# Kernel tuning notes

Measured on AMD Instinct MI355X. Metric: run time of the kernel, lower is better.

Reference implementation:

```python
import jax, jax.numpy as jnp
import numpy as np

V = 50000   # vocab_size
E = 300     # embed_dim (GRU input size)
H = 256     # hidden_dim
R = 2048    # number of replies
L0 = 128    # original content length
LR = 64     # max reply length (padded)

def setup_inputs() -> dict:
    key = jax.random.key(0)
    ks = jax.random.split(key, 20)
    s = 0.05
    inp = {
        "original_tokens": jax.random.randint(ks[0], (L0,), 0, V),
        "reply_tokens":    jax.random.randint(ks[1], (R, LR), 0, V),
        "reply_lengths":   jax.random.randint(ks[2], (R,), 1, LR + 1),
        "label":           jax.random.uniform(ks[3], (1,), dtype=jnp.float32),
        # learned params
        "embed": jax.random.normal(ks[4], (V, E), dtype=jnp.float32) * s,
        # bi-GRU forward direction (PyTorch layout: gates [r, z, n] stacked)
        "Wih_f": jax.random.normal(ks[5], (3 * H, E), dtype=jnp.float32) * s,
        "Whh_f": jax.random.normal(ks[6], (3 * H, H), dtype=jnp.float32) * s,
        "bih_f": jax.random.normal(ks[7], (3 * H,), dtype=jnp.float32) * s,
        "bhh_f": jax.random.normal(ks[8], (3 * H,), dtype=jnp.float32) * s,
        # bi-GRU reverse direction
        "Wih_b": jax.random.normal(ks[9], (3 * H, E), dtype=jnp.float32) * s,
        "Whh_b": jax.random.normal(ks[10], (3 * H, H), dtype=jnp.float32) * s,
        "bih_b": jax.random.normal(ks[11], (3 * H,), dtype=jnp.float32) * s,
        "bhh_b": jax.random.normal(ks[12], (3 * H,), dtype=jnp.float32) * s,
        # self.linear : 2H -> H
        "Wl": jax.random.normal(ks[13], (H, 2 * H), dtype=jnp.float32) * s,
        "bl": jax.random.normal(ks[14], (H,), dtype=jnp.float32) * s,
        # self.output_linear : H -> 1 (batch_size = 1)
        "Wo": jax.random.normal(ks[15], (1, H), dtype=jnp.float32) * s,
        "bo": jax.random.normal(ks[16], (1,), dtype=jnp.float32) * s,
    }
    return inp


def _gru_dir(x, Wih, Whh, bih, bhh):
    """Single-direction GRU over x: (S, E) -> (ys: (S, H), hT: (H,)).
    PyTorch gate math: r,z,n with n = tanh(gi_n + r * gh_n)."""
    def step(h, xt):
        gi = Wih @ xt + bih            # (3H,)
        gh = Whh @ h + bhh             # (3H,)
        r = jax.nn.sigmoid(gi[:H] + gh[:H])
        z = jax.nn.sigmoid(gi[H:2 * H] + gh[H:2 * H])
        n = jnp.tanh(gi[2 * H:] + r * gh[2 * H:])
        h_new = (1.0 - z) * n + z * h
        return h_new, h_new
    h0 = jnp.zeros((H,), dtype=x.dtype)
    hT, ys = jax.lax.scan(step, h0, x)
    return ys, hT


def reference(original_tokens, reply_tokens, reply_lengths, label,
              embed, Wih_f, Whh_f, bih_f, bhh_f,
              Wih_b, Whh_b, bih_b, bhh_b, Wl, bl, Wo, bo):
    # per-event embedding + sum pooling (batched replacement of Python loop)
    orig = embed[original_tokens].sum(axis=0)                      # (E,)
    mask = (jnp.arange(LR)[None, :] < reply_lengths[:, None]).astype(embed.dtype)
    rep = jnp.einsum('rle,rl->re', embed[reply_tokens], mask)      # (R, E)
    X = jnp.concatenate([orig[None, :], rep], axis=0)              # (S, E), S = R+1

    # bidirectional GRU (batch dim is 1, squeezed)
    ys_f, h_f = _gru_dir(X, Wih_f, Whh_f, bih_f, bhh_f)            # (S, H), (H,)
    ys_b, h_b = _gru_dir(X[::-1], Wih_b, Whh_b, bih_b, bhh_b)
    ys_b = ys_b[::-1]                                              # (S, H)

    out2 = jnp.concatenate([ys_f, ys_b], axis=-1)                  # (S, 2H)
    output = out2 @ Wl.T + bl                                      # (S, H)

    # hidden = sum over directions of final hidden states
    hsum = h_f + h_b                                               # (H,)

    # dot-product attention: query = hsum, keys = values = output
    scores = output @ hsum                                         # (S,)
    w = jax.nn.softmax(scores)                                     # attention dist
    ctx = w @ output                                               # (H,)

    result = jax.nn.sigmoid(ctx @ Wo.T + bo)                       # (1,)
    loss = (label - result) ** 2                                   # (1,)
    return (output[:, None, :], loss, result)                      # output: (S,1,H)
```

## Files before the change

kernel.cpp:

```cpp
#include <hip/hip_runtime.h>
#include <cstdint>
#include <cstddef>

#define NV 50000
#define NE 300
#define NH 256
#define NR 2048
#define NL0 128
#define NLR 64
#define NS 2049
#define G3 768

static constexpr size_t alignUp(size_t x, size_t a) { return (x + a - 1) / a * a; }
static constexpr size_t OFF_HCOM_F = 0;
static constexpr size_t OFF_HCOM_B = 4096;
static constexpr size_t OFF_CTX    = 8192;
static constexpr size_t OFF_SCORES = 9216;
static constexpr size_t OFF_X      = alignUp(OFF_SCORES + (size_t)NS*4, 256);
static constexpr size_t OFF_GI_F   = alignUp(OFF_X + (size_t)NS*NE*4, 256);
static constexpr size_t OFF_GI_B   = alignUp(OFF_GI_F + (size_t)NS*G3*4, 256);
static constexpr size_t OFF_OUT2   = alignUp(OFF_GI_B + (size_t)NS*G3*4, 256);

__global__ __launch_bounds__(320) void embed_sum_kernel(
    const int* __restrict__ otok, const int* __restrict__ rtok,
    const int* __restrict__ rlen, const float* __restrict__ embed,
    float* __restrict__ X)
{
    const int b = blockIdx.x;
    const int e = threadIdx.x;
    if (e >= NE) return;
    float acc = 0.f;
    if (b == 0) {
        for (int t = 0; t < NL0; ++t) {
            int tok = otok[t];
            acc += embed[(size_t)tok * NE + e];
        }
    } else {
        const int r = b - 1;
        const int L = rlen[r];
        const int* tr = rtok + (size_t)r * NLR;
        for (int t = 0; t < L; ++t) {
            int tok = tr[t];
            acc += embed[(size_t)tok * NE + e];
        }
    }
    X[(size_t)b * NE + e] = acc;
}

__global__ __launch_bounds__(256) void gemm_abt(
    const float* __restrict__ A, const float* __restrict__ B,
    const float* __restrict__ bias, float* __restrict__ C,
    int M, int N, int K, int ldc)
{
    __shared__ float As[16][65];
    __shared__ float Bs[16][65];
    const int bm = blockIdx.x * 64, bn = blockIdx.y * 64;
    const int tid = threadIdx.x;
    const int tx = tid & 15, ty = tid >> 4;
    float acc[4][4] = {};
    for (int k0 = 0; k0 < K; k0 += 16) {
        #pragma unroll
        for (int i = 0; i < 4; ++i) {
            int l = tid + 256 * i;
            int mm = l >> 4, kk = l & 15;
            int gm = bm + mm, gk = k0 + kk;
            As[kk][mm] = (gm < M && gk < K) ? A[(size_t)gm * K + gk] : 0.f;
            int gn = bn + mm;
            Bs[kk][mm] = (gk < K) ? B[(size_t)gn * K + gk] : 0.f;
        }
        __syncthreads();
        #pragma unroll
        for (int kk = 0; kk < 16; ++kk) {
            float a0 = As[kk][ty], a1 = As[kk][ty+16], a2 = As[kk][ty+32], a3 = As[kk][ty+48];
            float b0 = Bs[kk][tx], b1 = Bs[kk][tx+16], b2 = Bs[kk][tx+32], b3 = Bs[kk][tx+48];
            acc[0][0] += a0*b0; acc[0][1] += a0*b1; acc[0][2] += a0*b2; acc[0][3] += a0*b3;
            acc[1][0] += a1*b0; acc[1][1] += a1*b1; acc[1][2] += a1*b2; acc[1][3] += a1*b3;
            acc[2][0] += a2*b0; acc[2][1] += a2*b1; acc[2][2] += a2*b2; acc[2][3] += a2*b3;
            acc[3][0] += a3*b0; acc[3][1] += a3*b1; acc[3][2] += a3*b2; acc[3][3] += a3*b3;
        }
        __syncthreads();
    }
    #pragma unroll
    for (int i = 0; i < 4; ++i) {
        int gm = bm + ty + 16 * i;
        if (gm >= M) continue;
        #pragma unroll
        for (int j = 0; j < 4; ++j) {
            int gn = bn + tx + 16 * j;
            C[(size_t)gm * ldc + gn] = acc[i][j] + bias[gn];
        }
    }
}

__global__ __launch_bounds__(256) void gru_kernel(
    const float* __restrict__ Whh_f, const float* __restrict__ bhh_f,
    const float* __restrict__ Whh_b, const float* __restrict__ bhh_b,
    const float* __restrict__ gi_f, const float* __restrict__ gi_b,
    float* __restrict__ out2,
    unsigned long long* __restrict__ hcom_f,
    unsigned long long* __restrict__ hcom_b)
{
    const int dir = blockIdx.x >> 4;
    const int w   = blockIdx.x & 15;
    const int tid = threadIdx.x;

    const float* Whh = dir ? Whh_b : Whh_f;
    const float* bhh = dir ? bhh_b : bhh_f;
    const float* gi  = dir ? gi_b  : gi_f;
    unsigned long long* hcom = dir ? hcom_b : hcom_f;

    __shared__ float4 wP[64 * 49 + 48];
    __shared__ float4 h4[64];
    __shared__ float  ghs[48];
    __shared__ float  bh[48];
    float* h_s = (float*)h4;

    for (int idx = tid; idx < 48 * 64; idx += 256) {
        int lr = idx % 48, k4 = idx / 48;
        int g = ((lr >> 4) << 8) + (w << 4) + (lr & 15);
        wP[k4 * 49 + lr] = *(const float4*)(Whh + (size_t)g * NH + (k4 << 2));
    }
    if (tid < 48) {
        int g = ((tid >> 4) << 8) + (w << 4) + (tid & 15);
        bh[tid] = bhh[g];
    }
    h_s[tid] = 0.f;
    __syncthreads();

    for (int t = 0; t < NS; ++t) {
        const int s = dir ? (NS - 1 - t) : t;
        float gir = 0.f, giz = 0.f, gin = 0.f;
        if (tid >= 192 && tid < 208) {
            int i = tid - 192;
            const float* grow = gi + (size_t)s * G3 + (w << 4) + i;
            gir = grow[0]; giz = grow[NH]; gin = grow[2 * NH];
        }
        if (tid < 192) {
            int lr = tid >> 2, q = tid & 3;
            float acc = 0.f;
            #pragma unroll
            for (int i = 0; i < 16; ++i) {
                int k4 = (i << 2) + q;
                float4 wv = wP[k4 * 49 + lr];
                float4 hv = h4[k4];
                acc += wv.x * hv.x + wv.y * hv.y + wv.z * hv.z + wv.w * hv.w;
            }
            acc += __shfl_xor(acc, 1);
            acc += __shfl_xor(acc, 2);
            if (q == 0) ghs[lr] = acc + bh[lr];
        }
        __syncthreads();
        if (tid >= 192 && tid < 208) {
            int i = tid - 192;
            float r  = 1.f / (1.f + __expf(-(gir + ghs[i])));
            float z  = 1.f / (1.f + __expf(-(giz + ghs[16 + i])));
            float n  = tanhf(gin + r * ghs[32 + i]);
            float hn = (1.f - z) * n + z * h_s[(w << 4) + i];
            out2[(size_t)s * (2 * NH) + dir * NH + (w << 4) + i] = hn;
            unsigned long long pv =
                ((unsigned long long)(unsigned)(t + 1) << 32) |
                (unsigned long long)__float_as_uint(hn);
            __hip_atomic_store(&hcom[((t & 1) << 8) + (w << 4) + i], pv,
                               __ATOMIC_RELAXED, __HIP_MEMORY_SCOPE_AGENT);
            h_s[(w << 4) + i] = hn;
        }
        if (t < NS - 1 && (tid >> 4) != w) {
            const unsigned want = (unsigned)(t + 1);
            const int slot = ((t & 1) << 8) + tid;
            unsigned long long v;
            do {
                v = __hip_atomic_load(&hcom[slot], __ATOMIC_RELAXED, __HIP_MEMORY_SCOPE_AGENT);
            } while ((unsigned)(v >> 32) != want);
            h_s[tid] = __uint_as_float((unsigned)v);
        }
        __syncthreads();
    }
}

__global__ __launch_bounds__(256) void scores_kernel(
    const float* __restrict__ outp, const float* __restrict__ out2,
    float* __restrict__ scores)
{
    const int s = blockIdx.x, m = threadIdx.x;
    float hs = out2[(size_t)(NS - 1) * (2 * NH) + m] + out2[NH + m];
    float v = outp[(size_t)s * NH + m] * hs;
    #pragma unroll
    for (int o = 32; o > 0; o >>= 1) v += __shfl_down(v, o);
    __shared__ float p[4];
    if ((m & 63) == 0) p[m >> 6] = v;
    __syncthreads();
    if (m == 0) scores[s] = p[0] + p[1] + p[2] + p[3];
}

__global__ __launch_bounds__(1024) void softmax_kernel(float* __restrict__ sc)
{
    const int tid = threadIdx.x;
    __shared__ float red[16];
    float x0 = (tid < NS) ? sc[tid] : -3.0e38f;
    float x1 = (tid + 1024 < NS) ? sc[tid + 1024] : -3.0e38f;
    float mx = fmaxf(x0, x1);
    #pragma unroll
    for (int o = 32; o > 0; o >>= 1) mx = fmaxf(mx, __shfl_xor(mx, o));
    if ((tid & 63) == 0) red[tid >> 6] = mx;
    __syncthreads();
    if (tid == 0) {
        float m = red[0];
        for (int i = 1; i < 16; ++i) m = fmaxf(m, red[i]);
        red[0] = m;
    }
    __syncthreads();
    const float gmax = red[0];
    float e0 = (tid < NS) ? __expf(x0 - gmax) : 0.f;
    float e1 = (tid + 1024 < NS) ? __expf(x1 - gmax) : 0.f;
    float sm = e0 + e1;
    #pragma unroll
    for (int o = 32; o > 0; o >>= 1) sm += __shfl_xor(sm, o);
    __syncthreads();
    if ((tid & 63) == 0) red[tid >> 6] = sm;
    __syncthreads();
    if (tid == 0) {
        float su = 0.f;
        for (int i = 0; i < 16; ++i) su += red[i];
        red[1] = 1.f / su;
    }
    __syncthreads();
    const float inv = red[1];
    if (tid < NS) sc[tid] = e0 * inv;
    if (tid + 1024 < NS) sc[tid + 1024] = e1 * inv;
}

__global__ __launch_bounds__(256) void ctx_kernel(
    const float* __restrict__ outp, const float* __restrict__ w,
    float* __restrict__ ctx)
{
    const int m = threadIdx.x;
    const int s0 = blockIdx.x * 128;
    const int s1 = min(s0 + 128, NS);
    float acc = 0.f;
    for (int s = s0; s < s1; ++s) acc += w[s] * outp[(size_t)s * NH + m];
    atomicAdd(&ctx[m], acc);
}

__global__ __launch_bounds__(256) void final_kernel(
    const float* __restrict__ ctx, const float* __restrict__ Wo,
    const float* __restrict__ bo, const float* __restrict__ label,
    float* __restrict__ dout)
{
    const int m = threadIdx.x;
    float v = ctx[m] * Wo[m];
    #pragma unroll
    for (int o = 32; o > 0; o >>= 1) v += __shfl_down(v, o);
    __shared__ float p[4];
    if ((m & 63) == 0) p[m >> 6] = v;
    __syncthreads();
    if (m == 0) {
        float x = p[0] + p[1] + p[2] + p[3] + bo[0];
        float result = 1.f / (1.f + __expf(-x));
        float d = label[0] - result;
        dout[(size_t)NS * NH]     = d * d;
        dout[(size_t)NS * NH + 1] = result;
    }
}

extern "C" void kernel_launch(void* const* d_in, const int* in_sizes, int n_in,
                              void* d_out, int out_size, void* d_ws, size_t ws_size,
                              hipStream_t stream)
{
    const int*   otok  = (const int*)d_in[0];
    const int*   rtok  = (const int*)d_in[1];
    const int*   rlen  = (const int*)d_in[2];
    const float* label = (const float*)d_in[3];
    const float* embed = (const float*)d_in[4];
    const float* Wih_f = (const float*)d_in[5];
    const float* Whh_f = (const float*)d_in[6];
    const float* bih_f = (const float*)d_in[7];
    const float* bhh_f = (const float*)d_in[8];
    const float* Wih_b = (const float*)d_in[9];
    const float* Whh_b = (const float*)d_in[10];
    const float* bih_b = (const float*)d_in[11];
    const float* bhh_b = (const float*)d_in[12];
    const float* Wl    = (const float*)d_in[13];
    const float* bl    = (const float*)d_in[14];
    const float* Wo    = (const float*)d_in[15];
    const float* bo    = (const float*)d_in[16];

    char* ws = (char*)d_ws;
    unsigned long long* hcom_f = (unsigned long long*)(ws + OFF_HCOM_F);
    unsigned long long* hcom_b = (unsigned long long*)(ws + OFF_HCOM_B);
    float* ctx    = (float*)(ws + OFF_CTX);
    float* scores = (float*)(ws + OFF_SCORES);
    float* X      = (float*)(ws + OFF_X);
    float* gi_f   = (float*)(ws + OFF_GI_F);
    float* gi_b   = (float*)(ws + OFF_GI_B);
    float* out2   = (float*)(ws + OFF_OUT2);
    float* outp   = (float*)d_out;

    hipMemsetAsync(d_ws, 0, 9216, stream);

    embed_sum_kernel<<<NS, 320, 0, stream>>>(otok, rtok, rlen, embed, X);

    gemm_abt<<<dim3(33, 12), 256, 0, stream>>>(X, Wih_f, bih_f, gi_f, NS, G3, NE, G3);
    gemm_abt<<<dim3(33, 12), 256, 0, stream>>>(X, Wih_b, bih_b, gi_b, NS, G3, NE, G3);

    gru_kernel<<<32, 256, 0, stream>>>(Whh_f, bhh_f, Whh_b, bhh_b,
                                       gi_f, gi_b, out2, hcom_f, hcom_b);

    gemm_abt<<<dim3(33, 4), 256, 0, stream>>>(out2, Wl, bl, outp, NS, NH, 2 * NH, NH);

    scores_kernel<<<NS, 256, 0, stream>>>(outp, out2, scores);
    softmax_kernel<<<1, 1024, 0, stream>>>(scores);
    ctx_kernel<<<(NS + 127) / 128, 256, 0, stream>>>(outp, scores, ctx);
    final_kernel<<<1, 256, 0, stream>>>(ctx, Wo, bo, label, (float*)d_out);
}
```

Measured before the change: 3.439 ms.

## Restructure GRU recurrence into 8 blocks per direction with per-block mailboxes

The recurrent GRU kernel now uses 8 workgroups of 512 threads per direction instead of 16 of 256. The recurrent weights are held in registers rather than shared memory, and every compute thread computes all three gates for its hidden element. Each block sends its new hidden state to a dedicated mailbox slot per consumer block, and a separate half of the threads spin on and collect incoming values. The next step's input-gate values are prefetched, and a single raw barrier replaces two __syncthreads per step. The intent is to cut per-step latency on the serial recurrence, at the cost of heavy register pressure and more cross-block traffic per block.

Result: no change. 3.395 ms (-1.3%).

```diff
diff --git a/kernel.cpp b/kernel.cpp
--- a/kernel.cpp
+++ b/kernel.cpp
@@ -10,16 +10,18 @@
 #define NLR 64
 #define NS 2049
 #define G3 768
+#define NWG 8
+#define EPW 32
 
 static constexpr size_t alignUp(size_t x, size_t a) { return (x + a - 1) / a * a; }
-static constexpr size_t OFF_HCOM_F = 0;
-static constexpr size_t OFF_HCOM_B = 4096;
-static constexpr size_t OFF_CTX    = 8192;
-static constexpr size_t OFF_SCORES = 9216;
-static constexpr size_t OFF_X      = alignUp(OFF_SCORES + (size_t)NS*4, 256);
-static constexpr size_t OFF_GI_F   = alignUp(OFF_X + (size_t)NS*NE*4, 256);
-static constexpr size_t OFF_GI_B   = alignUp(OFF_GI_F + (size_t)NS*G3*4, 256);
-static constexpr size_t OFF_OUT2   = alignUp(OFF_GI_B + (size_t)NS*G3*4, 256);
+static constexpr size_t OFF_MAIL   = 0;
+static constexpr size_t MAIL_U64S  = 2ull * 2 * NWG * NH;
+static constexpr size_t OFF_CTX    = OFF_MAIL + MAIL_U64S * 8;
+static constexpr size_t OFF_SCORES = OFF_CTX + 1024;
+static constexpr size_t OFF_X      = alignUp(OFF_SCORES + (size_t)NS * 4, 256);
+static constexpr size_t OFF_GI_F   = alignUp(OFF_X + (size_t)NS * NE * 4, 256);
+static constexpr size_t OFF_GI_B   = alignUp(OFF_GI_F + (size_t)NS * G3 * 4, 256);
+static constexpr size_t OFF_OUT2   = alignUp(OFF_GI_B + (size_t)NS * G3 * 4, 256);
 
 __global__ __launch_bounds__(320) void embed_sum_kernel(
     const int* __restrict__ otok, const int* __restrict__ rtok,
@@ -92,88 +94,101 @@
     }
 }
 
-__global__ __launch_bounds__(256) void gru_kernel(
+__global__ __launch_bounds__(512) void gru_kernel(
     const float* __restrict__ Whh_f, const float* __restrict__ bhh_f,
     const float* __restrict__ Whh_b, const float* __restrict__ bhh_b,
     const float* __restrict__ gi_f, const float* __restrict__ gi_b,
     float* __restrict__ out2,
-    unsigned long long* __restrict__ hcom_f,
-    unsigned long long* __restrict__ hcom_b)
-{
-    const int dir = blockIdx.x >> 4;
-    const int w   = blockIdx.x & 15;
+    unsigned long long* __restrict__ mail)
+{
+    const int dir = blockIdx.x >> 3;
+    const int w   = blockIdx.x & 7;
     const int tid = threadIdx.x;
 
-    const float* Whh = dir ? Whh_b : Whh_f;
-    const float* bhh = dir ? bhh_b : bhh_f;
-    const float* gi  = dir ? gi_b  : gi_f;
-    unsigned long long* hcom = dir ? hcom_b : hcom_f;
-
-    __shared__ float4 wP[64 * 49 + 48];
-    __shared__ float4 h4[64];
-    __shared__ float  ghs[48];
-    __shared__ float  bh[48];
-    float* h_s = (float*)h4;
-
-    for (int idx = tid; idx < 48 * 64; idx += 256) {
-        int lr = idx % 48, k4 = idx / 48;
-        int g = ((lr >> 4) << 8) + (w << 4) + (lr & 15);
-        wP[k4 * 49 + lr] = *(const float4*)(Whh + (size_t)g * NH + (k4 << 2));
-    }
-    if (tid < 48) {
-        int g = ((tid >> 4) << 8) + (w << 4) + (tid & 15);
-        bh[tid] = bhh[g];
-    }
-    h_s[tid] = 0.f;
+    const float* __restrict__ Whh = dir ? Whh_b : Whh_f;
+    const float* __restrict__ bhh = dir ? bhh_b : bhh_f;
+    const float* __restrict__ gi  = dir ? gi_b  : gi_f;
+    unsigned long long* __restrict__ mbase = mail + (size_t)dir * (2 * NWG * NH);
+
+    __shared__ __align__(16) float hbuf[2][NH];
+
+    if (tid < NH) hbuf[0][tid] = 0.f;
+
+    float4 wr[8], wz[8], wn[8];
+    float bhr = 0.f, bhz = 0.f, bhn = 0.f;
+    float gir = 0.f, giz = 0.f, gin = 0.f;
+    int e = 0, j = 0;
+
+    if (tid < 256) {
+        e = w * EPW + (tid >> 3);
+        j = tid & 7;
+        const float* r0 = Whh + (size_t)e * NH;
+        const float* r1 = Whh + (size_t)(NH + e) * NH;
+        const float* r2 = Whh + (size_t)(2 * NH + e) * NH;
+        #pragma unroll
+        for (int c = 0; c < 8; ++c) {
+            int off = c * 32 + j * 4;
+            wr[c] = *(const float4*)(r0 + off);
+            wz[c] = *(const float4*)(r1 + off);
+            wn[c] = *(const float4*)(r2 + off);
+        }
+        bhr = bhh[e]; bhz = bhh[NH + e]; bhn = bhh[2 * NH + e];
+        const float* g0 = gi + (size_t)(dir ? NS - 1 : 0) * G3 + e;
+        gir = g0[0]; giz = g0[NH]; gin = g0[2 * NH];
+    }
     __syncthreads();
 
     for (int t = 0; t < NS; ++t) {
-        const int s = dir ? (NS - 1 - t) : t;
-        float gir = 0.f, giz = 0.f, gin = 0.f;
-        if (tid >= 192 && tid < 208) {
-            int i = tid - 192;
-            const float* grow = gi + (size_t)s * G3 + (w << 4) + i;
-            gir = grow[0]; giz = grow[NH]; gin = grow[2 * NH];
-        }
-        if (tid < 192) {
-            int lr = tid >> 2, q = tid & 3;
-            float acc = 0.f;
+        const int p = t & 1;
+        if (tid < 256) {
+            const int s = dir ? (NS - 1 - t) : t;
+            float girN = 0.f, gizN = 0.f, ginN = 0.f;
+            if (t < NS - 1) {
+                const float* gn = gi + (size_t)(dir ? (NS - 2 - t) : (t + 1)) * G3 + e;
+                girN = gn[0]; gizN = gn[NH]; ginN = gn[2 * NH];
+            }
+            const float hprev = hbuf[p][e];
+            const float4* hq = (const float4*)hbuf[p];
+            float ar = 0.f, az = 0.f, an = 0.f;
             #pragma unroll
-            for (int i = 0; i < 16; ++i) {
-                int k4 = (i << 2) + q;
-                float4 wv = wP[k4 * 49 + lr];
-                float4 hv = h4[k4];
-                acc += wv.x * hv.x + wv.y * hv.y + wv.z * hv.z + wv.w * hv.w;
+            for (int c = 0; c < 8; ++c) {
+                float4 h4 = hq[c * 8 + j];
+                ar += wr[c].x*h4.x + wr[c].y*h4.y + wr[c].z*h4.z + wr[c].w*h4.w;
+                az += wz[c].x*h4.x + wz[c].y*h4.y + wz[c].z*h4.z + wz[c].w*h4.w;
+                an += wn[c].x*h4.x + wn[c].y*h4.y + wn[c].z*h4.z + wn[c].w*h4.w;
             }
-            acc += __shfl_xor(acc, 1);
-            acc += __shfl_xor(acc, 2);
-            if (q == 0) ghs[lr] = acc + bh[lr];
-        }
-        __syncthreads();
-        if (tid >= 192 && tid < 208) {
-            int i = tid - 192;
-            float r  = 1.f / (1.f + __expf(-(gir + ghs[i])));
-            float z  = 1.f / (1.f + __expf(-(giz + ghs[16 + i])));
-            float n  = tanhf(gin + r * ghs[32 + i]);
-            float hn = (1.f - z) * n + z * h_s[(w << 4) + i];
-            out2[(size_t)s * (2 * NH) + dir * NH + (w << 4) + i] = hn;
-            unsigned long long pv =
-                ((unsigned long long)(unsigned)(t + 1) << 32) |
-                (unsigned long long)__float_as_uint(hn);
-            __hip_atomic_store(&hcom[((t & 1) << 8) + (w << 4) + i], pv,
-                               __ATOMIC_RELAXED, __HIP_MEMORY_SCOPE_AGENT);
-            h_s[(w << 4) + i] = hn;
-        }
-        if (t < NS - 1 && (tid >> 4) != w) {
-            const unsigned want = (unsigned)(t + 1);
-            const int slot = ((t & 1) << 8) + tid;
-            unsigned long long v;
-            do {
-                v = __hip_atomic_load(&hcom[slot], __ATOMIC_RELAXED, __HIP_MEMORY_SCOPE_AGENT);
-            } while ((unsigned)(v >> 32) != want);
-            h_s[tid] = __uint_as_float((unsigned)v);
-        }
-        __syncthreads();
+            ar += __shfl_xor(ar, 1); az += __shfl_xor(az, 1); an += __shfl_xor(an, 1);
+            ar += __shfl_xor(ar, 2); az += __shfl_xor(az, 2); an += __shfl_xor(an, 2);
+            ar += __shfl_xor(ar, 4); az += __shfl_xor(az, 4); an += __shfl_xor(an, 4);
+            const float r  = 1.f / (1.f + __expf(-(gir + ar + bhr)));
+            const float z  = 1.f / (1.f + __expf(-(giz + az + bhz)));
+            const float n  = tanhf(gin + r * (an + bhn));
+            const float hn = (1.f - z) * n + z * hprev;
+            if (t < NS - 1) {
+                if (j != w) {
+                    unsigned long long pv =
+                        ((unsigned long long)(unsigned)(t + 1) << 32) |
+                        (unsigned long long)__float_as_uint(hn);
+                    __hip_atomic_store(&mbase[((size_t)p * NWG + j) * NH + e], pv,
+                                       __ATOMIC_RELAXED, __HIP_MEMORY_SCOPE_AGENT);
+                }
+                if (j == 0) hbuf[p ^ 1][e] = hn;
+            }
+            if (j == 0) out2[(size_t)s * (2 * NH) + dir * NH + e] = hn;
+            gir = girN; giz = gizN; gin = ginN;
+        } else {
+            const int slot = tid - 256;
+            if (t < NS - 1 && (slot >> 5) != w) {
+                const unsigned want = (unsigned)(t + 1);
+                unsigned long long v;
+                do {
+                    v = __hip_atomic_load(&mbase[((size_t)p * NWG + w) * NH + slot],
+                                          __ATOMIC_RELAXED, __HIP_MEMORY_SCOPE_AGENT);
+                } while ((unsigned)(v >> 32) != want);
+                hbuf[p ^ 1][slot] = __uint_as_float((unsigned)v);
+            }
+        }
+        asm volatile("s_waitcnt lgkmcnt(0)\n\ts_barrier" ::: "memory");
     }
 }
 
@@ -285,8 +300,7 @@
     const float* bo    = (const float*)d_in[16];
 
     char* ws = (char*)d_ws;
-    unsigned long long* hcom_f = (unsigned long long*)(ws + OFF_HCOM_F);
-    unsigned long long* hcom_b = (unsigned long long*)(ws + OFF_HCOM_B);
+    unsigned long long* mail = (unsigned long long*)(ws + OFF_MAIL);
     float* ctx    = (float*)(ws + OFF_CTX);
     float* scores = (float*)(ws + OFF_SCORES);
     float* X      = (float*)(ws + OFF_X);
@@ -295,15 +309,15 @@
     float* out2   = (float*)(ws + OFF_OUT2);
     float* outp   = (float*)d_out;
 
-    hipMemsetAsync(d_ws, 0, 9216, stream);
+    hipMemsetAsync(d_ws, 0, OFF_SCORES, stream);
 
     embed_sum_kernel<<<NS, 320, 0, stream>>>(otok, rtok, rlen, embed, X);
 
     gemm_abt<<<dim3(33, 12), 256, 0, stream>>>(X, Wih_f, bih_f, gi_f, NS, G3, NE, G3);
     gemm_abt<<<dim3(33, 12), 256, 0, stream>>>(X, Wih_b, bih_b, gi_b, NS, G3, NE, G3);
 
-    gru_kernel<<<32, 256, 0, stream>>>(Whh_f, bhh_f, Whh_b, bhh_b,
-                                       gi_f, gi_b, out2, hcom_f, hcom_b);
+    gru_kernel<<<16, 512, 0, stream>>>(Whh_f, bhh_f, Whh_b, bhh_b,
+                                       gi_f, gi_b, out2, mail);
 
     gemm_abt<<<dim3(33, 4), 256, 0, stream>>>(out2, Wl, bl, outp, NS, NH, 2 * NH, NH);
 
```
